# Optimization experiments

Hardware: AMD Instinct MI355X
Metric: run time of the kernel (lower is better)

The kernel has to match this reference:

```python
import jax, jax.numpy as jnp
import numpy as np
from jax.scipy.special import logsumexp

# config constants (match init_kwargs)
EPS_SH, IT_SH = 0.05, 10      # shared-space sinkhorn
EPS_AN, IT_AN = 0.05, 10      # anchor-space sinkhorn
TEMP_SAIL, BIAS_SAIL = 10.0, 0.0
CLAMP = 1e-8


def _rownorm(x):
    return x / jnp.clip(jnp.linalg.norm(x, axis=1, keepdims=True), CLAMP)


def cosine_similarity_matrix(a, b):
    return _rownorm(a) @ _rownorm(b).T


def sinkhorn(dist, epsilon, max_iter):
    """Log-domain Sinkhorn with uniform marginals. dist: (nx, ny)."""
    nx, ny = dist.shape
    M = -dist / epsilon                      # (nx, ny) log kernel
    log_a = -jnp.log(jnp.float32(nx))
    log_b = -jnp.log(jnp.float32(ny))

    def step(carry, _):
        u, v = carry
        u = log_a - logsumexp(M + v[None, :], axis=1)
        v = log_b - logsumexp(M + u[:, None], axis=0)
        return (u, v), None

    init = (jnp.zeros((nx,), M.dtype), jnp.zeros((ny,), M.dtype))
    (u, v), _ = jax.lax.scan(step, init, None, length=max_iter)
    log_plan = M + u[:, None] + v[None, :]
    return jnp.exp(log_plan), log_plan


def setup_inputs() -> dict:
    key = jax.random.key(0)
    ks = jax.random.split(key, 8)
    return {
        "fX_pairs": jax.random.normal(ks[0], (2048, 256), jnp.float32),
        "fY_pairs": jax.random.normal(ks[1], (2048, 256), jnp.float32),
        "X":        jax.random.normal(ks[2], (4096, 768), jnp.float32),
        "Y":        jax.random.normal(ks[3], (4096, 512), jnp.float32),
        "fX":       jax.random.normal(ks[4], (4096, 256), jnp.float32),
        "fY":       jax.random.normal(ks[5], (4096, 256), jnp.float32),
        "X_anchor": jax.random.normal(ks[6], (4096, 768), jnp.float32),
        "Y_anchor": jax.random.normal(ks[7], (4096, 512), jnp.float32),
    }


def _forward(fX_pairs, fY_pairs, X, Y, fX, fY, X_anchor, Y_anchor):
    # --- anchor covariances ---
    Xa, Ya = _rownorm(X_anchor), _rownorm(Y_anchor)
    Na = jnp.float32(Xa.shape[0])
    Sxx = (Xa.T @ Xa) / Na
    Syy = (Ya.T @ Ya) / Na
    Sxy = (Xa.T @ Ya) / Na

    # --- latent-space transport plans (shared sinkhorn) ---
    plan_p, logp_p = sinkhorn(-cosine_similarity_matrix(fX_pairs, fY_pairs), EPS_SH, IT_SH)
    plan_u, logp_u = sinkhorn(-cosine_similarity_matrix(fX, fY), EPS_SH, IT_SH)

    # --- marginal loss: marginals should be uniform ---
    def marginal_loss(plan):
        nx, ny = plan.shape
        a = jnp.full((nx,), 1.0 / nx, plan.dtype)
        b = jnp.full((ny,), 1.0 / ny, plan.dtype)
        return ((plan.sum(1) - a) ** 2).sum() + ((plan.sum(0) - b) ** 2).sum()

    L_marg = marginal_loss(plan_p) + marginal_loss(plan_u)

    # --- SAIL sigmoid contrastive loss on pairs ---
    N = fX_pairs.shape[0]
    cos = cosine_similarity_matrix(fX_pairs, fY_pairs)
    target = -1.0 + 2.0 * jnp.eye(N, dtype=cos.dtype)
    L_sail = -jnp.mean(jax.nn.log_sigmoid(cos * TEMP_SAIL * target - BIAS_SAIL))

    # --- supervised explicit: cosine distance on pairs ---
    L_exp = jnp.mean((1.0 - (_rownorm(fX_pairs) * _rownorm(fY_pairs)).sum(-1)) / 2.0)

    # --- supervised implicit: diag of log plan vs uniform identity ---
    L_imp = -jnp.mean(jnp.diag(logp_p) + jnp.log(jnp.float32(N)))

    # --- anchor-space plan (torch.no_grad -> stop_gradient) ---
    nX = jnp.clip(jnp.sqrt((X * (X @ Sxx)).sum(-1, keepdims=True)), CLAMP)
    nY = jnp.clip(jnp.sqrt((Y * (Y @ Syy)).sum(-1, keepdims=True)), CLAMP)
    Xn, Yn = X / nX, Y / nY
    plan_a, logp_a = jax.lax.stop_gradient(sinkhorn(-(Xn @ Sxy @ Yn.T), EPS_AN, IT_AN))
    Xn = jax.lax.stop_gradient(Xn)
    Yn = jax.lax.stop_gradient(Yn)

    # --- semisupervised OT: KL(plan_anchor || plan_latent) ---
    L_ot = (plan_a * (logp_a - logp_u)).sum()

    # --- semisupervised divergence (frobenius) ---
    fXn, fYn = _rownorm(fX), _rownorm(fY)
    norm1 = (((Xn.T @ Xn) @ Sxy @ (Yn.T @ Yn)) * Sxy).sum()
    norm2 = ((fXn.T @ fXn) * (fYn.T @ fYn)).sum()
    dot = (((Xn.T @ fXn) @ (fYn.T @ Yn)) * Sxy).sum()
    cste = jnp.float32(X.shape[0] * Y.shape[0])
    L_div = (norm1 + norm2 - 2.0 * dot) / cste

    # --- unsupervised Gromov-Wasserstein-style loss ---
    Xu = jax.lax.stop_gradient(_rownorm(X))
    Yu = jax.lax.stop_gradient(_rownorm(Y))
    Kx = Xu @ Xu.T   # (Nx, Nx)
    Ky = Yu @ Yu.T   # (Ny, Ny)
    a = plan_u.sum(1)
    b = plan_u.sum(0)
    L_gw = (a @ (Kx ** 2) @ a + b @ (Ky ** 2) @ b
            - 2.0 * ((Kx @ plan_u @ Ky) * plan_u).sum())

    return L_marg + L_sail + L_exp + L_imp + L_ot + L_div + L_gw


def reference(fX_pairs, fY_pairs, X, Y, fX, fY, X_anchor, Y_anchor):
    return _forward(fX_pairs, fY_pairs, X, Y, fX, fY, X_anchor, Y_anchor)
```

## Files before the change

### kernel.cpp

```cpp
#include <hip/hip_runtime.h>
#include <hip/hip_bf16.h>
#include <math.h>

using u16 = unsigned short;
using s8v = __attribute__((ext_vector_type(8))) short;
using s4v = __attribute__((ext_vector_type(4))) short;
using f4v = __attribute__((ext_vector_type(4))) float;

__device__ __forceinline__ float b2f(u16 x) {
    unsigned int u = ((unsigned int)x) << 16;
    return __uint_as_float(u);
}
__device__ __forceinline__ u16 f2b(float f) {
    unsigned int x = __float_as_uint(f);
    unsigned int r = x + 0x7fffu + ((x >> 16) & 1u);
    return (u16)(r >> 16);
}

__device__ __forceinline__ void a16(u16* lds, const u16* g) {
    __builtin_amdgcn_global_load_lds((__attribute__((address_space(1))) void*)g,
                                     (__attribute__((address_space(3))) void*)lds,
                                     16, 0, 0);
}

__device__ __forceinline__ float block_sum(float v, float* buf) {
    int t = threadIdx.x;
    buf[t] = v; __syncthreads();
    for (int s = 128; s > 0; s >>= 1) {
        if (t < s) buf[t] += buf[t + s];
        __syncthreads();
    }
    float r = buf[0];
    __syncthreads();
    return r;
}

__device__ __forceinline__ float wave_sum(float v) {
#pragma unroll
    for (int off = 32; off; off >>= 1) v += __shfl_xor(v, off, 64);
    return v;
}

__device__ __forceinline__ void block_atomic4(float wval, float* slot) {
    __shared__ float wb[4];
    int lane = threadIdx.x & 63, wv = threadIdx.x >> 6;
    if (lane == 0) wb[wv] = wval;
    __syncthreads();
    if (threadIdx.x == 0) atomicAdd(slot, wb[0] + wb[1] + wb[2] + wb[3]);
}

#define TBM 128
#define TBN 128
#define TBK 32

template<int EPI>
__global__ __launch_bounds__(256)
void gemm_bt(const u16* __restrict__ A, const u16* __restrict__ B,
             float* __restrict__ Cf, u16* __restrict__ Cb,
             int M, int N, int K, int ld, float alpha)
{
    __shared__ __align__(16) u16 As[TBM * TBK];
    __shared__ __align__(16) u16 Bs[TBN * TBK];

    const int tid  = threadIdx.x;
    const int lane = tid & 63;
    const int wave = tid >> 6;
    const int wm   = (wave >> 1) * 64;
    const int wn   = (wave & 1) * 64;
    const int l16  = lane & 15;
    const int q4   = lane >> 4;
    const size_t row0 = (size_t)blockIdx.y * TBM;
    const size_t col0 = (size_t)blockIdx.x * TBN;
    const int kOff = blockIdx.z * K;

    f4v acc[4][4];
#pragma unroll
    for (int mt = 0; mt < 4; ++mt)
#pragma unroll
        for (int nt = 0; nt < 4; ++nt)
#pragma unroll
            for (int r = 0; r < 4; ++r)
                acc[mt][nt][r] = 0.f;

    const int ar0 = wave * 32 + (lane >> 2);
    const int ar1 = ar0 + 16;
    const int akk = (lane & 3) * 8;
    const u16* gA0 = A + (row0 + ar0) * ld + kOff + akk;
    const u16* gA1 = A + (row0 + ar1) * ld + kOff + akk;
    const u16* gB0 = B + (col0 + ar0) * ld + kOff + akk;
    const u16* gB1 = B + (col0 + ar1) * ld + kOff + akk;
    u16* lA0 = As + wave * 1024;
    u16* lA1 = As + wave * 1024 + 512;
    u16* lB0 = Bs + wave * 1024;
    u16* lB1 = Bs + wave * 1024 + 512;

    for (int k0 = 0; k0 < K; k0 += TBK) {
        __syncthreads();
        a16(lA0, gA0 + k0);
        a16(lA1, gA1 + k0);
        a16(lB0, gB0 + k0);
        a16(lB1, gB1 + k0);
        __syncthreads();

        s8v af[4], bfr[4];
#pragma unroll
        for (int mt = 0; mt < 4; ++mt)
            af[mt] = *(const s8v*)(As + (wm + mt * 16 + l16) * TBK + q4 * 8);
#pragma unroll
        for (int nt = 0; nt < 4; ++nt)
            bfr[nt] = *(const s8v*)(Bs + (wn + nt * 16 + l16) * TBK + q4 * 8);
#pragma unroll
        for (int mt = 0; mt < 4; ++mt)
#pragma unroll
            for (int nt = 0; nt < 4; ++nt)
                acc[mt][nt] = __builtin_amdgcn_mfma_f32_16x16x32_bf16(af[mt], bfr[nt], acc[mt][nt], 0, 0, 0);
    }

#pragma unroll
    for (int mt = 0; mt < 4; ++mt)
#pragma unroll
        for (int nt = 0; nt < 4; ++nt)
#pragma unroll
            for (int r = 0; r < 4; ++r) {
                size_t row = row0 + wm + mt * 16 + q4 * 4 + r;
                size_t col = col0 + wn + nt * 16 + l16;
                float v = acc[mt][nt][r] * alpha;
                if (EPI == 1) Cb[row * (size_t)N + col] = f2b(v);
                else          atomicAdd(&Cf[row * (size_t)N + col], v);
            }
}

struct BGN {
    const u16* A; const u16* B;
    float* Cf; u16* Cb;
    const u16* W; float* slot;
    int M, N, Kc, ld, WL, tN, tEnd;
};
struct BGNArgs { BGN d[6]; int n; float alpha; };

template<int EPI>
__global__ __launch_bounds__(256)
void bgemmN(BGNArgs g)
{
    __shared__ __align__(16) u16 As[TBM * TBK];
    __shared__ __align__(16) u16 Bs[TBN * TBK];

    int bi = 0;
    while (bi < g.n - 1 && (int)blockIdx.x >= g.d[bi].tEnd) ++bi;
    const BGN& d = g.d[bi];
    const int tStart = bi ? g.d[bi - 1].tEnd : 0;
    const int local = blockIdx.x - tStart;
    const int tm = local / d.tN;
    const int tn = local - tm * d.tN;

    const int tid  = threadIdx.x;
    const int lane = tid & 63;
    const int wave = tid >> 6;
    const int wm   = (wave >> 1) * 64;
    const int wn   = (wave & 1) * 64;
    const int l16  = lane & 15;
    const int q4   = lane >> 4;
    const size_t row0 = (size_t)tm * TBM;
    const size_t col0 = (size_t)tn * TBN;
    const int kOff = blockIdx.y * d.Kc;
    const int ld = d.ld;

    f4v acc[4][4];
#pragma unroll
    for (int mt = 0; mt < 4; ++mt)
#pragma unroll
        for (int nt = 0; nt < 4; ++nt)
#pragma unroll
            for (int r = 0; r < 4; ++r)
                acc[mt][nt][r] = 0.f;

    const int ar0 = wave * 32 + (lane >> 2);
    const int ar1 = ar0 + 16;
    const int akk = (lane & 3) * 8;
    const u16* gA0 = d.A + (row0 + ar0) * ld + kOff + akk;
    const u16* gA1 = d.A + (row0 + ar1) * ld + kOff + akk;
    const u16* gB0 = d.B + (col0 + ar0) * ld + kOff + akk;
    const u16* gB1 = d.B + (col0 + ar1) * ld + kOff + akk;
    u16* lA0 = As + wave * 1024;
    u16* lA1 = As + wave * 1024 + 512;
    u16* lB0 = Bs + wave * 1024;
    u16* lB1 = Bs + wave * 1024 + 512;

    for (int k0 = 0; k0 < d.Kc; k0 += TBK) {
        __syncthreads();
        a16(lA0, gA0 + k0);
        a16(lA1, gA1 + k0);
        a16(lB0, gB0 + k0);
        a16(lB1, gB1 + k0);
        __syncthreads();

        s8v af[4], bfr[4];
#pragma unroll
        for (int mt = 0; mt < 4; ++mt)
            af[mt] = *(const s8v*)(As + (wm + mt * 16 + l16) * TBK + q4 * 8);
#pragma unroll
        for (int nt = 0; nt < 4; ++nt)
            bfr[nt] = *(const s8v*)(Bs + (wn + nt * 16 + l16) * TBK + q4 * 8);
#pragma unroll
        for (int mt = 0; mt < 4; ++mt)
#pragma unroll
            for (int nt = 0; nt < 4; ++nt)
                acc[mt][nt] = __builtin_amdgcn_mfma_f32_16x16x32_bf16(af[mt], bfr[nt], acc[mt][nt], 0, 0, 0);
    }

    if (EPI == 2) {
        float local2 = 0.f;
#pragma unroll
        for (int mt = 0; mt < 4; ++mt)
#pragma unroll
            for (int nt = 0; nt < 4; ++nt)
#pragma unroll
                for (int r = 0; r < 4; ++r) {
                    size_t row = row0 + wm + mt * 16 + q4 * 4 + r;
                    size_t col = col0 + wn + nt * 16 + l16;
                    local2 += acc[mt][nt][r] * b2f(d.W[col * (size_t)d.WL + row]);
                }
        __shared__ float red[256];
        float tot = block_sum(local2 * g.alpha, red);
        if (tid == 0) atomicAdd(d.slot, tot);
    } else {
#pragma unroll
        for (int mt = 0; mt < 4; ++mt)
#pragma unroll
            for (int nt = 0; nt < 4; ++nt)
#pragma unroll
                for (int r = 0; r < 4; ++r) {
                    size_t row = row0 + wm + mt * 16 + q4 * 4 + r;
                    size_t col = col0 + wn + nt * 16 + l16;
                    float v = acc[mt][nt][r] * g.alpha;
                    if (EPI == 0)      d.Cf[row * (size_t)d.N + col] = v;
                    else if (EPI == 1) d.Cb[row * (size_t)d.N + col] = f2b(v);
                    else               atomicAdd(&d.Cf[row * (size_t)d.N + col], v);
                }
    }
}

struct RN { const float* in; u16* out; int C; int rEnd; };
struct RNArgs { RN d[8]; int n; };

__global__ __launch_bounds__(256)
void rownorm_batch(RNArgs a) {
    int gw = (blockIdx.x * 256 + threadIdx.x) >> 6;
    int lane = threadIdx.x & 63;
    int i = 0;
    while (i < a.n - 1 && gw >= a.d[i].rEnd) ++i;
    if (gw >= a.d[i].rEnd) return;
    int row = gw - (i ? a.d[i - 1].rEnd : 0);
    int C = a.d[i].C;
    const float4* r4 = (const float4*)(a.d[i].in + (size_t)row * C);
    int nv = C >> 2;
    float ss = 0.f;
    for (int c = lane; c < nv; c += 64) {
        float4 v = r4[c];
        ss += v.x * v.x + v.y * v.y + v.z * v.z + v.w * v.w;
    }
    ss = wave_sum(ss);
    float inv = 1.f / fmaxf(sqrtf(ss), 1e-8f);
    s4v* o4 = (s4v*)(a.d[i].out + (size_t)row * C);
    for (int c = lane; c < nv; c += 64) {
        float4 v = r4[c];
        s4v o;
        o[0] = (short)f2b(v.x * inv); o[1] = (short)f2b(v.y * inv);
        o[2] = (short)f2b(v.z * inv); o[3] = (short)f2b(v.w * inv);
        o4[c] = o;
    }
}

__global__ __launch_bounds__(256)
void mahal_w(const u16* __restrict__ Xh, const float* __restrict__ XS,
             u16* __restrict__ out, int nrows, int C) {
    int row = (blockIdx.x * 256 + threadIdx.x) >> 6;
    int lane = threadIdx.x & 63;
    if (row >= nrows) return;
    const s4v* x4 = (const s4v*)(Xh + (size_t)row * C);
    const float4* s4 = (const float4*)(XS + (size_t)row * C);
    int nv = C >> 2;
    float s = 0.f;
    for (int c = lane; c < nv; c += 64) {
        s4v x = x4[c]; float4 v = s4[c];
        s += b2f((u16)x[0]) * v.x + b2f((u16)x[1]) * v.y
           + b2f((u16)x[2]) * v.z + b2f((u16)x[3]) * v.w;
    }
    s = wave_sum(s);
    float inv = 1.f / fmaxf(sqrtf(fmaxf(s, 0.f)), 1e-8f);
    s4v* o4 = (s4v*)(out + (size_t)row * C);
    for (int c = lane; c < nv; c += 64) {
        s4v x = x4[c], o;
#pragma unroll
        for (int k = 0; k < 4; ++k) o[k] = (short)f2b(b2f((u16)x[k]) * inv);
        o4[c] = o;
    }
}

struct TP { const u16* in; u16* out; int R, C, tC, tEnd; const float* s; };
struct TPArgs { TP d[6]; int n; };

__global__ __launch_bounds__(256)
void transpose_batch(TPArgs a) {
    __shared__ u16 tile[32][33];
    int t = blockIdx.x;
    int i = 0;
    while (i < a.n - 1 && t >= a.d[i].tEnd) ++i;
    int local = t - (i ? a.d[i - 1].tEnd : 0);
    const TP& d = a.d[i];
    int ty = local / d.tC, tx = local - ty * d.tC;
    int bx = tx * 32, by = ty * 32;
    int lx = threadIdx.x & 31;
    int lyy = threadIdx.x >> 5;
    for (int r = lyy; r < 32; r += 8)
        tile[r][lx] = d.in[(size_t)(by + r) * d.C + bx + lx];
    __syncthreads();
    for (int r = lyy; r < 32; r += 8) {
        u16 val = tile[lx][r];
        if (d.s) val = f2b(b2f(val) * d.s[by + lx]);
        d.out[(size_t)(bx + r) * d.R + by + lx] = val;
    }
}

__global__ __launch_bounds__(256)
void cast_f2b(const float* __restrict__ in, u16* __restrict__ out, int n) {
    for (int i = blockIdx.x * 256 + threadIdx.x; i < n; i += gridDim.x * 256)
        out[i] = f2b(in[i]);
}

__device__ __forceinline__ float row_sumexp(const u16* __restrict__ rowp,
                                            const float* __restrict__ vin,
                                            int ny, float scale, int lane) {
    const s8v* r8 = (const s8v*)rowp;
    const float4* v4 = (const float4*)vin;
    int nv = ny >> 3;
    float s = 0.f;
    for (int c = lane; c < nv; c += 64) {
        s8v v8 = r8[c];
        float4 va = v4[c * 2], vb = v4[c * 2 + 1];
        s += __expf(b2f((u16)v8[0]) * scale + va.x);
        s += __expf(b2f((u16)v8[1]) * scale + va.y);
        s += __expf(b2f((u16)v8[2]) * scale + va.z);
        s += __expf(b2f((u16)v8[3]) * scale + va.w);
        s += __expf(b2f((u16)v8[4]) * scale + vb.x);
        s += __expf(b2f((u16)v8[5]) * scale + vb.y);
        s += __expf(b2f((u16)v8[6]) * scale + vb.z);
        s += __expf(b2f((u16)v8[7]) * scale + vb.w);
    }
    return wave_sum(s);
}

__global__ __launch_bounds__(256)
void row_lse_tri(const u16* __restrict__ C1, const float* __restrict__ v1, float* __restrict__ u1,
                 const u16* __restrict__ C2, const float* __restrict__ v2, float* __restrict__ u2,
                 const u16* __restrict__ C3, const float* __restrict__ v3, float* __restrict__ u3,
                 float scale, float lm12, float lm3) {
    int gw = (blockIdx.x * 256 + threadIdx.x) >> 6;
    int lane = threadIdx.x & 63;
    if (gw < 4096) {
        float s = row_sumexp(C1 + (size_t)gw * 4096, v1, 4096, scale, lane);
        if (lane == 0) u1[gw] = lm12 - __logf(s);
    } else if (gw < 8192) {
        int row = gw - 4096;
        float s = row_sumexp(C2 + (size_t)row * 4096, v2, 4096, scale, lane);
        if (lane == 0) u2[row] = lm12 - __logf(s);
    } else {
        int row = gw - 8192;
        if (row >= 2048) return;
        float s = row_sumexp(C3 + (size_t)row * 2048, v3, 2048, scale, lane);
        if (lane == 0) u3[row] = lm3 - __logf(s);
    }
}

__device__ __forceinline__ float plan_body(const u16* __restrict__ rowp, u16* __restrict__ prow,
                                           float ui, const float* __restrict__ vin,
                                           int ny, float scale, int lane) {
    const s8v* r8 = (const s8v*)rowp;
    s8v* p8 = (s8v*)prow;
    const float4* v4 = (const float4*)vin;
    int nv = ny >> 3;
    float s = 0.f;
    for (int c = lane; c < nv; c += 64) {
        s8v v8 = r8[c], pb;
        float4 va = v4[c * 2], vb = v4[c * 2 + 1];
        float vv[8] = {va.x, va.y, va.z, va.w, vb.x, vb.y, vb.z, vb.w};
#pragma unroll
        for (int k = 0; k < 8; ++k) {
            float p = __expf(b2f((u16)v8[k]) * scale + ui + vv[k]);
            s += p;
            pb[k] = (short)f2b(p);
        }
        if (p8) p8[c] = pb;
    }
    return wave_sum(s);
}

__global__ __launch_bounds__(256)
void plan_quad(const u16* __restrict__ Cu, const u16* __restrict__ CuT,
               const u16* __restrict__ cosp, const u16* __restrict__ cospT,
               const float* __restrict__ uu, const float* __restrict__ vu,
               const float* __restrict__ up, const float* __restrict__ vp,
               u16* __restrict__ plan,
               float* __restrict__ au, float* __restrict__ bu,
               float* __restrict__ ap, float* __restrict__ bp, float scale) {
    int gw = (blockIdx.x * 256 + threadIdx.x) >> 6;
    int lane = threadIdx.x & 63;
    if (gw < 4096) {
        float s = plan_body(Cu + (size_t)gw * 4096, plan + (size_t)gw * 4096, uu[gw], vu, 4096, scale, lane);
        if (lane == 0) au[gw] = s;
    } else if (gw < 8192) {
        int r = gw - 4096;
        float s = plan_body(CuT + (size_t)r * 4096, nullptr, vu[r], uu, 4096, scale, lane);
        if (lane == 0) bu[r] = s;
    } else if (gw < 10240) {
        int r = gw - 8192;
        float s = plan_body(cosp + (size_t)r * 2048, nullptr, up[r], vp, 2048, scale, lane);
        if (lane == 0) ap[r] = s;
    } else {
        int r = gw - 10240;
        if (r >= 2048) return;
        float s = plan_body(cospT + (size_t)r * 2048, nullptr, vp[r], up, 2048, scale, lane);
        if (lane == 0) bp[r] = s;
    }
}

__global__ __launch_bounds__(256)
void marg4(const float* __restrict__ ap, const float* __restrict__ bp,
           const float* __restrict__ au, const float* __restrict__ bu,
           float* __restrict__ slot) {
    const float* sv; int n; float target;
    if (blockIdx.x == 0)      { sv = ap; n = 2048; target = 1.f / 2048.f; }
    else if (blockIdx.x == 1) { sv = bp; n = 2048; target = 1.f / 2048.f; }
    else if (blockIdx.x == 2) { sv = au; n = 4096; target = 1.f / 4096.f; }
    else                      { sv = bu; n = 4096; target = 1.f / 4096.f; }
    int t = threadIdx.x;
    float s = 0.f;
    for (int i = t; i < n; i += 256) { float d = sv[i] - target; s += d * d; }
    __shared__ float buf[256];
    float tot = block_sum(s, buf);
    if (t == 0) atomicAdd(slot, tot);
}

__global__ __launch_bounds__(256)
void ot_row_w(const u16* __restrict__ Ca, const u16* __restrict__ Cu,
              const float* __restrict__ ua, const float* __restrict__ va,
              const float* __restrict__ uu, const float* __restrict__ vu,
              int nrows, int ny, float scale, float* __restrict__ slot) {
    int row = (blockIdx.x * 256 + threadIdx.x) >> 6;
    int lane = threadIdx.x & 63;
    float local = 0.f;
    if (row < nrows) {
        const s8v* ra = (const s8v*)(Ca + (size_t)row * ny);
        const s8v* ru = (const s8v*)(Cu + (size_t)row * ny);
        const float4* va4 = (const float4*)va;
        const float4* vu4 = (const float4*)vu;
        float uai = ua[row], uui = uu[row];
        int nv = ny >> 3;
        for (int c = lane; c < nv; c += 64) {
            s8v a8 = ra[c], u8 = ru[c];
            float4 a0 = va4[c * 2], a1 = va4[c * 2 + 1];
            float4 u0 = vu4[c * 2], u1 = vu4[c * 2 + 1];
            float av[8] = {a0.x, a0.y, a0.z, a0.w, a1.x, a1.y, a1.z, a1.w};
            float uv[8] = {u0.x, u0.y, u0.z, u0.w, u1.x, u1.y, u1.z, u1.w};
#pragma unroll
            for (int k = 0; k < 8; ++k) {
                float lpa = b2f((u16)a8[k]) * scale + uai + av[k];
                float lpu = b2f((u16)u8[k]) * scale + uui + uv[k];
                local += __expf(lpa) * (lpa - lpu);
            }
        }
    }
    local = wave_sum(local);
    block_atomic4(local, slot);
}

__global__ __launch_bounds__(256)
void sail_row_w(const u16* __restrict__ cosb, int n, float temp, float* __restrict__ slot) {
    int row = (blockIdx.x * 256 + threadIdx.x) >> 6;
    int lane = threadIdx.x & 63;
    float local = 0.f;
    if (row < n) {
        const s8v* r8 = (const s8v*)(cosb + (size_t)row * n);
        int nv = n >> 3;
        for (int c = lane; c < nv; c += 64) {
            s8v v8 = r8[c];
#pragma unroll
            for (int k = 0; k < 8; ++k) {
                int j = c * 8 + k;
                float cv = b2f((u16)v8[k]);
                float wgt = cv * ((j == row) ? temp : -temp);
                local -= fminf(wgt, 0.f) - log1pf(__expf(-fabsf(wgt)));
            }
        }
    }
    local = wave_sum(local);
    block_atomic4(local, slot);
}

__global__ __launch_bounds__(256)
void diag2(const u16* __restrict__ cosb, const float* __restrict__ up,
           const float* __restrict__ vp, int n, float scale,
           float* __restrict__ slotExp, float* __restrict__ slotImp) {
    int t = threadIdx.x;
    float e = 0.f, im = 0.f;
    float logn = logf((float)n);
    for (int i = t; i < n; i += 256) {
        float c = b2f(cosb[(size_t)i * n + i]);
        e  += (1.f - c) * 0.5f;
        im += scale * c + up[i] + vp[i] + logn;
    }
    __shared__ float buf[256];
    float te = block_sum(e, buf);
    float ti = block_sum(im, buf);
    if (t == 0) { atomicAdd(slotExp, te); atomicAdd(slotImp, ti); }
}

__global__ __launch_bounds__(256)
void dot_bb(const u16* __restrict__ A, const u16* __restrict__ B, int n,
            float* __restrict__ slot) {
    int t = threadIdx.x;
    float local = 0.f;
    for (int i = blockIdx.x * 256 + t; i < n; i += gridDim.x * 256)
        local += b2f(A[i]) * b2f(B[i]);
    __shared__ float buf[256];
    float tot = block_sum(local, buf);
    if (t == 0) atomicAdd(slot, tot);
}

__global__ __launch_bounds__(256)
void dot3(const float* __restrict__ A, const float* __restrict__ B, const float* __restrict__ C,
          int na, int nb, int nc, float* __restrict__ sA, float* __restrict__ sB, float* __restrict__ sC) {
    const float* p; int n, b0, nblk; float* slot;
    if (blockIdx.x < 32)      { p = A; n = na; b0 = 0;  nblk = 32; slot = sA; }
    else if (blockIdx.x < 48) { p = B; n = nb; b0 = 32; nblk = 16; slot = sB; }
    else                      { p = C; n = nc; b0 = 48; nblk = 16; slot = sC; }
    int t = threadIdx.x;
    float local = 0.f;
    for (int i = (blockIdx.x - b0) * 256 + t; i < n; i += nblk * 256) {
        float v = p[i]; local += v * v;
    }
    __shared__ float buf[256];
    float tot = block_sum(local, buf);
    if (t == 0) atomicAdd(slot, tot);
}

__global__ void combine(const float* __restrict__ s, float* __restrict__ out) {
    if (threadIdx.x == 0 && blockIdx.x == 0) {
        float Np = 2048.f;
        float Nu2 = 4096.f * 4096.f;
        float total = s[0]
                    + s[1] / (Np * Np)
                    + s[2] / Np
                    - s[3] / Np
                    + s[4]
                    + (s[5] + s[6] - 2.f * s[7]) / Nu2
                    + s[8] + s[9] - 2.f * s[10];
        out[0] = total;
    }
}

extern "C" void kernel_launch(void* const* d_in, const int* in_sizes, int n_in,
                              void* d_out, int out_size, void* d_ws, size_t ws_size,
                              hipStream_t stream) {
    const float* fXp_in = (const float*)d_in[0];
    const float* fYp_in = (const float*)d_in[1];
    const float* X_in   = (const float*)d_in[2];
    const float* Y_in   = (const float*)d_in[3];
    const float* fX_in  = (const float*)d_in[4];
    const float* fY_in  = (const float*)d_in[5];
    const float* Xa_in  = (const float*)d_in[6];
    const float* Ya_in  = (const float*)d_in[7];
    float* out = (float*)d_out;

    char* w = (char*)d_ws;
    size_t off = 0;
    auto alloc = [&](size_t bytes) -> char* {
        char* p = w + off;
        off += (bytes + 255) & ~(size_t)255;
        return p;
    };

    const size_t N = 4096, Np = 2048, DX = 768, DY = 512, DF = 256;

    const size_t SLOT = N * N * 2;
    char* S1 = alloc(SLOT);
    char* S2 = alloc(SLOT);
    char* S3 = alloc(SLOT);
    char* S4 = alloc(SLOT);
    char* S5 = alloc(SLOT);

    u16* Xa   = (u16*)S1;
    u16* Cu   = (u16*)S1;
    u16* T1T  = (u16*)S1;
    u16* Ya   = (u16*)S2;
    u16* CuT  = (u16*)S2;
    u16* XuT  = (u16*)S2;
    u16* YuT  = (u16*)(S2 + N * DX * 2);
    u16* Ca   = (u16*)S3;
    u16* XsT  = (u16*)S3;
    u16* YsT  = (u16*)(S3 + N * DX * 2);
    u16* XaT  = (u16*)S4;
    u16* YaT  = (u16*)(S4 + N * DX * 2);
    float* XS = (float*)S4;
    u16* XnT  = (u16*)S4;
    u16* YnT  = (u16*)(S4 + N * DX * 2);
    u16* CaT  = (u16*)S4;
    float* T1F= (float*)S4;
    float* YS = (float*)S5;
    u16* Tb   = (u16*)S5;
    u16* plan = (u16*)S5;

    u16* fXp  = (u16*)alloc(Np * DF * 2);
    u16* fYp  = (u16*)alloc(Np * DF * 2);
    u16* fXn  = (u16*)alloc(N * DF * 2);
    u16* fYn  = (u16*)alloc(N * DF * 2);
    u16* fXnT = (u16*)alloc(N * DF * 2);
    u16* fYnT = (u16*)alloc(N * DF * 2);
    u16* Xu   = (u16*)alloc(N * DX * 2);
    u16* Yu   = (u16*)alloc(N * DY * 2);
    u16* Xn   = (u16*)alloc(N * DX * 2);
    u16* Yn   = (u16*)alloc(N * DY * 2);
    u16* Sxx  = (u16*)alloc(DX * DX * 2);
    u16* Syy  = (u16*)alloc(DY * DY * 2);
    u16* SxyT = (u16*)alloc(DY * DX * 2);
    u16* Gx   = (u16*)alloc(DX * DX * 2);
    u16* Gy   = (u16*)alloc(DY * DY * 2);
    u16* Gfx  = (u16*)alloc(DF * DF * 2);
    u16* Gfy  = (u16*)alloc(DF * DF * 2);
    u16* A1b  = (u16*)alloc(DX * DF * 2);
    u16* B1Tb = (u16*)alloc(DY * DF * 2);
    u16* Hb   = (u16*)alloc(DX * DY * 2);
    u16* cosp = (u16*)alloc(Np * Np * 2);
    u16* cospT= (u16*)alloc(Np * Np * 2);
    float* ap = (float*)alloc(Np * 4);
    float* bp = (float*)alloc(Np * 4);
    float* au = (float*)alloc(N * 4);
    float* bu = (float*)alloc(N * 4);

    char* zero_begin = w + off;
    float* slots = (float*)alloc(64 * 4);
    float* up = (float*)alloc(Np * 4);
    float* vp = (float*)alloc(Np * 4);
    float* uu = (float*)alloc(N * 4);
    float* vu = (float*)alloc(N * 4);
    float* ua = (float*)alloc(N * 4);
    float* va = (float*)alloc(N * 4);
    float* SxxF  = (float*)alloc(DX * DX * 4);
    float* SyyF  = (float*)alloc(DY * DY * 4);
    float* SxyTF = (float*)alloc(DY * DX * 4);
    float* GxF   = (float*)alloc(DX * DX * 4);
    float* GyF   = (float*)alloc(DY * DY * 4);
    float* GfxF  = (float*)alloc(DF * DF * 4);
    float* GfyF  = (float*)alloc(DF * DF * 4);
    float* A1F   = (float*)alloc(DX * DF * 4);
    float* B1F   = (float*)alloc(DY * DF * 4);
    float* HbF   = (float*)alloc(DX * DY * 4);
    float* W1F   = (float*)alloc(DX * DX * 4);
    float* W2F   = (float*)alloc(DY * DY * 4);
    float* MF    = (float*)alloc(DX * DY * 4);
    size_t zero_bytes = (size_t)((w + off) - zero_begin);

    const float SCALE = 20.f;

    hipMemsetAsync(zero_begin, 0, zero_bytes, stream);

    {
        RNArgs a;
        a.d[0] = {Xa_in, Xa, 768, 4096};
        a.d[1] = {Ya_in, Ya, 512, 8192};
        a.d[2] = {fXp_in, fXp, 256, 10240};
        a.d[3] = {fYp_in, fYp, 256, 12288};
        a.d[4] = {fX_in, fXn, 256, 16384};
        a.d[5] = {fY_in, fYn, 256, 20480};
        a.d[6] = {X_in, Xu, 768, 24576};
        a.d[7] = {Y_in, Yu, 512, 28672};
        a.n = 8;
        rownorm_batch<<<7168, 256, 0, stream>>>(a);
    }

    {
        TPArgs a;
        a.d[0] = {Xa, XaT, 4096, 768, 24, 3072, nullptr};
        a.d[1] = {Ya, YaT, 4096, 512, 16, 5120, nullptr};
        a.d[2] = {fXn, fXnT, 4096, 256, 8, 6144, nullptr};
        a.d[3] = {fYn, fYnT, 4096, 256, 8, 7168, nullptr};
        a.n = 4;
        transpose_batch<<<7168, 256, 0, stream>>>(a);
    }

    {
        BGNArgs g;
        g.d[0] = {XaT, XaT, SxxF, nullptr, nullptr, nullptr, 768, 768, 512, 4096, 0, 6, 36};
        g.d[1] = {YaT, YaT, SyyF, nullptr, nullptr, nullptr, 512, 512, 512, 4096, 0, 4, 52};
        g.d[2] = {YaT, XaT, SxyTF, nullptr, nullptr, nullptr, 512, 768, 512, 4096, 0, 6, 76};
        g.n = 3; g.alpha = 1.f / 4096.f;
        bgemmN<3><<<dim3(76, 8), 256, 0, stream>>>(g);
        cast_f2b<<<256, 256, 0, stream>>>(SxxF, Sxx, 768 * 768 + 512 * 512 + 512 * 768);
    }

    {
        BGNArgs g;
        g.d[0] = {Xu, Sxx, XS, nullptr, nullptr, nullptr, 4096, 768, 768, 768, 0, 6, 192};
        g.d[1] = {Yu, Syy, YS, nullptr, nullptr, nullptr, 4096, 512, 512, 512, 0, 4, 320};
        g.n = 2; g.alpha = 1.f;
        bgemmN<0><<<dim3(320, 1), 256, 0, stream>>>(g);
    }
    mahal_w<<<1024, 256, 0, stream>>>(Xu, XS, Xn, 4096, 768);
    mahal_w<<<1024, 256, 0, stream>>>(Yu, YS, Yn, 4096, 512);

    {
        TPArgs a;
        a.d[0] = {Xn, XnT, 4096, 768, 24, 3072, nullptr};
        a.d[1] = {Yn, YnT, 4096, 512, 16, 5120, nullptr};
        a.n = 2;
        transpose_batch<<<5120, 256, 0, stream>>>(a);
    }

    {
        BGNArgs g;
        g.d[0] = {XnT, XnT, GxF, nullptr, nullptr, nullptr, 768, 768, 512, 4096, 0, 6, 36};
        g.d[1] = {YnT, YnT, GyF, nullptr, nullptr, nullptr, 512, 512, 512, 4096, 0, 4, 52};
        g.d[2] = {fXnT, fXnT, GfxF, nullptr, nullptr, nullptr, 256, 256, 512, 4096, 0, 2, 56};
        g.d[3] = {fYnT, fYnT, GfyF, nullptr, nullptr, nullptr, 256, 256, 512, 4096, 0, 2, 60};
        g.d[4] = {XnT, fXnT, A1F, nullptr, nullptr, nullptr, 768, 256, 512, 4096, 0, 2, 72};
        g.d[5] = {YnT, fYnT, B1F, nullptr, nullptr, nullptr, 512, 256, 512, 4096, 0, 2, 80};
        g.n = 6; g.alpha = 1.f;
        bgemmN<3><<<dim3(80, 8), 256, 0, stream>>>(g);
        cast_f2b<<<256, 256, 0, stream>>>(GxF, Gx,
            768 * 768 + 512 * 512 + 256 * 256 + 256 * 256 + 768 * 256 + 512 * 256);
    }

    {
        BGNArgs g;
        g.d[0] = {fXn, fYn, nullptr, Cu, nullptr, nullptr, 4096, 4096, 256, 256, 0, 32, 1024};
        g.d[1] = {fXp, fYp, nullptr, cosp, nullptr, nullptr, 2048, 2048, 256, 256, 0, 16, 1280};
        g.d[2] = {Xn, SxyT, nullptr, Tb, nullptr, nullptr, 4096, 512, 768, 768, 0, 4, 1408};
        g.n = 3; g.alpha = 1.f;
        bgemmN<1><<<dim3(1408, 1), 256, 0, stream>>>(g);
    }
    gemm_bt<1><<<dim3(32, 32), 256, 0, stream>>>(Tb, Yn, nullptr, Ca, 4096, 4096, 512, 512, 1.f);

    {
        TPArgs a;
        a.d[0] = {Cu, CuT, 4096, 4096, 128, 16384, nullptr};
        a.d[1] = {cosp, cospT, 2048, 2048, 64, 20480, nullptr};
        a.d[2] = {Ca, CaT, 4096, 4096, 128, 36864, nullptr};
        a.n = 3;
        transpose_batch<<<36864, 256, 0, stream>>>(a);
    }

    gemm_bt<3><<<dim3(4, 6, 4), 256, 0, stream>>>(Gx, SxyT, HbF, nullptr, 768, 512, 192, 768, 1.f);
    cast_f2b<<<256, 256, 0, stream>>>(HbF, Hb, 768 * 512);
    {
        BGNArgs g;
        g.d[0] = {Hb, Gy, nullptr, nullptr, SxyT, slots + 5, 768, 512, 128, 512, 768, 4, 24};
        g.d[1] = {A1b, B1Tb, nullptr, nullptr, SxyT, slots + 7, 768, 512, 64, 256, 768, 4, 48};
        g.n = 2; g.alpha = 1.f;
        bgemmN<2><<<dim3(48, 4), 256, 0, stream>>>(g);
    }
    dot_bb<<<64, 256, 0, stream>>>(Gfx, Gfy, 256 * 256, slots + 6);

    {
        float lm12 = -logf(4096.f), lm3 = -logf(2048.f);
        for (int it = 0; it < 10; ++it) {
            row_lse_tri<<<2560, 256, 0, stream>>>(Cu, vu, uu, Ca, va, ua, cosp, vp, up, SCALE, lm12, lm3);
            row_lse_tri<<<2560, 256, 0, stream>>>(CuT, uu, vu, CaT, ua, va, cospT, up, vp, SCALE, lm12, lm3);
        }
    }

    plan_quad<<<3072, 256, 0, stream>>>(Cu, CuT, cosp, cospT, uu, vu, up, vp,
                                        plan, au, bu, ap, bp, SCALE);
    marg4<<<4, 256, 0, stream>>>(ap, bp, au, bu, slots + 0);
    diag2<<<1, 256, 0, stream>>>(cosp, up, vp, 2048, SCALE, slots + 2, slots + 3);
    sail_row_w<<<512, 256, 0, stream>>>(cosp, 2048, 10.f, slots + 1);

    ot_row_w<<<1024, 256, 0, stream>>>(Ca, Cu, ua, va, uu, vu, 4096, 4096, SCALE, slots + 4);

    {
        TPArgs a;
        a.d[0] = {Xu, XuT, 4096, 768, 24, 3072, nullptr};
        a.d[1] = {Yu, YuT, 4096, 512, 16, 5120, nullptr};
        a.d[2] = {Xu, XsT, 4096, 768, 24, 8192, au};
        a.d[3] = {Yu, YsT, 4096, 512, 16, 10240, bu};
        a.n = 4;
        transpose_batch<<<10240, 256, 0, stream>>>(a);
    }
    hipMemsetAsync(T1F, 0, 512 * 4096 * 4, stream);
    {
        BGNArgs g;
        g.d[0] = {YuT, plan, T1F, nullptr, nullptr, nullptr, 512, 4096, 512, 4096, 0, 32, 128};
        g.d[1] = {XsT, XuT, W1F, nullptr, nullptr, nullptr, 768, 768, 512, 4096, 0, 6, 164};
        g.d[2] = {YsT, YuT, W2F, nullptr, nullptr, nullptr, 512, 512, 512, 4096, 0, 4, 180};
        g.n = 3; g.alpha = 1.f;
        bgemmN<3><<<dim3(180, 8), 256, 0, stream>>>(g);
    }
    cast_f2b<<<512, 256, 0, stream>>>(T1F, T1T, 512 * 4096);
    {
        BGNArgs g;
        g.d[0] = {XuT, T1T, MF, nullptr, nullptr, nullptr, 768, 512, 512, 4096, 0, 4, 24};
        g.n = 1; g.alpha = 1.f;
        bgemmN<3><<<dim3(24, 8), 256, 0, stream>>>(g);
    }
    dot3<<<64, 256, 0, stream>>>(W1F, W2F, MF, 768 * 768, 512 * 512, 768 * 512,
                                 slots + 8, slots + 9, slots + 10);

    combine<<<1, 1, 0, stream>>>(slots, out);
}
```

Baseline: 917.2 us.

## Fuse plan and OT passes, drop column marginals, split-K GEMMs into partial buffers

Merges the unsupervised plan computation with the OT KL row reduction so Cu is read once, and drops the column-sum passes over CuT/cospT along with their marginal terms. The GW split-K GEMMs now write per-slice partial results (new EPI 4) instead of atomically accumulating into a zeroed buffer. A new reduction kernel sums the partials, casts T1 to bf16 and computes the squared norms. The W2 path uses YuT directly with a 1/4096 scale rather than a b-weighted transpose. This assumes uniform column marginals (b = 1/N after the final v update), which holds for Sinkhorn ending on a v step, but it changes how the exact marginal error is computed and may be numerically approximate.

```diff
diff --git a/kernel.cpp b/kernel.cpp
--- a/kernel.cpp
+++ b/kernel.cpp
@@ -224,6 +224,7 @@
         float tot = block_sum(local2 * g.alpha, red);
         if (tid == 0) atomicAdd(d.slot, tot);
     } else {
+        float* Cs = (EPI == 4) ? d.Cf + (size_t)blockIdx.y * d.M * d.N : d.Cf;
 #pragma unroll
         for (int mt = 0; mt < 4; ++mt)
 #pragma unroll
@@ -235,6 +236,7 @@
                     float v = acc[mt][nt][r] * g.alpha;
                     if (EPI == 0)      d.Cf[row * (size_t)d.N + col] = v;
                     else if (EPI == 1) d.Cb[row * (size_t)d.N + col] = f2b(v);
+                    else if (EPI == 4) Cs[row * (size_t)d.N + col] = v;
                     else               atomicAdd(&d.Cf[row * (size_t)d.N + col], v);
                 }
     }
@@ -372,106 +374,77 @@
     }
 }
 
-__device__ __forceinline__ float plan_body(const u16* __restrict__ rowp, u16* __restrict__ prow,
-                                           float ui, const float* __restrict__ vin,
-                                           int ny, float scale, int lane) {
-    const s8v* r8 = (const s8v*)rowp;
-    s8v* p8 = (s8v*)prow;
-    const float4* v4 = (const float4*)vin;
-    int nv = ny >> 3;
-    float s = 0.f;
-    for (int c = lane; c < nv; c += 64) {
-        s8v v8 = r8[c], pb;
-        float4 va = v4[c * 2], vb = v4[c * 2 + 1];
-        float vv[8] = {va.x, va.y, va.z, va.w, vb.x, vb.y, vb.z, vb.w};
-#pragma unroll
-        for (int k = 0; k < 8; ++k) {
-            float p = __expf(b2f((u16)v8[k]) * scale + ui + vv[k]);
-            s += p;
-            pb[k] = (short)f2b(p);
-        }
-        if (p8) p8[c] = pb;
-    }
-    return wave_sum(s);
-}
-
-__global__ __launch_bounds__(256)
-void plan_quad(const u16* __restrict__ Cu, const u16* __restrict__ CuT,
-               const u16* __restrict__ cosp, const u16* __restrict__ cospT,
-               const float* __restrict__ uu, const float* __restrict__ vu,
-               const float* __restrict__ up, const float* __restrict__ vp,
-               u16* __restrict__ plan,
-               float* __restrict__ au, float* __restrict__ bu,
-               float* __restrict__ ap, float* __restrict__ bp, float scale) {
+__global__ __launch_bounds__(256)
+void plan_ot(const u16* __restrict__ Cu, const u16* __restrict__ Ca,
+             const u16* __restrict__ cosp,
+             const float* __restrict__ uu, const float* __restrict__ vu,
+             const float* __restrict__ ua, const float* __restrict__ va,
+             const float* __restrict__ up, const float* __restrict__ vp,
+             u16* __restrict__ plan,
+             float* __restrict__ au, float* __restrict__ ap,
+             float* __restrict__ slotOt, float scale) {
     int gw = (blockIdx.x * 256 + threadIdx.x) >> 6;
     int lane = threadIdx.x & 63;
-    if (gw < 4096) {
-        float s = plan_body(Cu + (size_t)gw * 4096, plan + (size_t)gw * 4096, uu[gw], vu, 4096, scale, lane);
-        if (lane == 0) au[gw] = s;
-    } else if (gw < 8192) {
+    if (blockIdx.x < 1024) {
+        int i = gw;
+        const s8v* ru = (const s8v*)(Cu + (size_t)i * 4096);
+        const s8v* ra = (const s8v*)(Ca + (size_t)i * 4096);
+        s8v* p8 = (s8v*)(plan + (size_t)i * 4096);
+        const float4* vu4 = (const float4*)vu;
+        const float4* va4 = (const float4*)va;
+        float uui = uu[i], uai = ua[i];
+        float sa = 0.f, ot = 0.f;
+        for (int c = lane; c < 512; c += 64) {
+            s8v u8 = ru[c], a8 = ra[c], pb;
+            float4 u0 = vu4[c * 2], u1 = vu4[c * 2 + 1];
+            float4 a0 = va4[c * 2], a1 = va4[c * 2 + 1];
+            float uv[8] = {u0.x, u0.y, u0.z, u0.w, u1.x, u1.y, u1.z, u1.w};
+            float av[8] = {a0.x, a0.y, a0.z, a0.w, a1.x, a1.y, a1.z, a1.w};
+#pragma unroll
+            for (int k = 0; k < 8; ++k) {
+                float lpu = b2f((u16)u8[k]) * scale + uui + uv[k];
+                float p = __expf(lpu);
+                sa += p;
+                pb[k] = (short)f2b(p);
+                float lpa = b2f((u16)a8[k]) * scale + uai + av[k];
+                ot += __expf(lpa) * (lpa - lpu);
+            }
+            p8[c] = pb;
+        }
+        sa = wave_sum(sa);
+        if (lane == 0) au[i] = sa;
+        ot = wave_sum(ot);
+        block_atomic4(ot, slotOt);
+    } else {
         int r = gw - 4096;
-        float s = plan_body(CuT + (size_t)r * 4096, nullptr, vu[r], uu, 4096, scale, lane);
-        if (lane == 0) bu[r] = s;
-    } else if (gw < 10240) {
-        int r = gw - 8192;
-        float s = plan_body(cosp + (size_t)r * 2048, nullptr, up[r], vp, 2048, scale, lane);
+        const s8v* r8 = (const s8v*)(cosp + (size_t)r * 2048);
+        const float4* vp4 = (const float4*)vp;
+        float ui = up[r], s = 0.f;
+        for (int c = lane; c < 256; c += 64) {
+            s8v v8 = r8[c];
+            float4 v0 = vp4[c * 2], v1 = vp4[c * 2 + 1];
+            float vv[8] = {v0.x, v0.y, v0.z, v0.w, v1.x, v1.y, v1.z, v1.w};
+#pragma unroll
+            for (int k = 0; k < 8; ++k)
+                s += __expf(b2f((u16)v8[k]) * scale + ui + vv[k]);
+        }
+        s = wave_sum(s);
         if (lane == 0) ap[r] = s;
-    } else {
-        int r = gw - 10240;
-        if (r >= 2048) return;
-        float s = plan_body(cospT + (size_t)r * 2048, nullptr, vp[r], up, 2048, scale, lane);
-        if (lane == 0) bp[r] = s;
-    }
-}
-
-__global__ __launch_bounds__(256)
-void marg4(const float* __restrict__ ap, const float* __restrict__ bp,
-           const float* __restrict__ au, const float* __restrict__ bu,
+    }
+}
+
+__global__ __launch_bounds__(256)
+void marg2(const float* __restrict__ ap, const float* __restrict__ au,
            float* __restrict__ slot) {
     const float* sv; int n; float target;
-    if (blockIdx.x == 0)      { sv = ap; n = 2048; target = 1.f / 2048.f; }
-    else if (blockIdx.x == 1) { sv = bp; n = 2048; target = 1.f / 2048.f; }
-    else if (blockIdx.x == 2) { sv = au; n = 4096; target = 1.f / 4096.f; }
-    else                      { sv = bu; n = 4096; target = 1.f / 4096.f; }
+    if (blockIdx.x == 0) { sv = ap; n = 2048; target = 1.f / 2048.f; }
+    else                 { sv = au; n = 4096; target = 1.f / 4096.f; }
     int t = threadIdx.x;
     float s = 0.f;
     for (int i = t; i < n; i += 256) { float d = sv[i] - target; s += d * d; }
     __shared__ float buf[256];
     float tot = block_sum(s, buf);
     if (t == 0) atomicAdd(slot, tot);
-}
-
-__global__ __launch_bounds__(256)
-void ot_row_w(const u16* __restrict__ Ca, const u16* __restrict__ Cu,
-              const float* __restrict__ ua, const float* __restrict__ va,
-              const float* __restrict__ uu, const float* __restrict__ vu,
-              int nrows, int ny, float scale, float* __restrict__ slot) {
-    int row = (blockIdx.x * 256 + threadIdx.x) >> 6;
-    int lane = threadIdx.x & 63;
-    float local = 0.f;
-    if (row < nrows) {
-        const s8v* ra = (const s8v*)(Ca + (size_t)row * ny);
-        const s8v* ru = (const s8v*)(Cu + (size_t)row * ny);
-        const float4* va4 = (const float4*)va;
-        const float4* vu4 = (const float4*)vu;
-        float uai = ua[row], uui = uu[row];
-        int nv = ny >> 3;
-        for (int c = lane; c < nv; c += 64) {
-            s8v a8 = ra[c], u8 = ru[c];
-            float4 a0 = va4[c * 2], a1 = va4[c * 2 + 1];
-            float4 u0 = vu4[c * 2], u1 = vu4[c * 2 + 1];
-            float av[8] = {a0.x, a0.y, a0.z, a0.w, a1.x, a1.y, a1.z, a1.w};
-            float uv[8] = {u0.x, u0.y, u0.z, u0.w, u1.x, u1.y, u1.z, u1.w};
-#pragma unroll
-            for (int k = 0; k < 8; ++k) {
-                float lpa = b2f((u16)a8[k]) * scale + uai + av[k];
-                float lpu = b2f((u16)u8[k]) * scale + uui + uv[k];
-                local += __expf(lpa) * (lpa - lpu);
-            }
-        }
-    }
-    local = wave_sum(local);
-    block_atomic4(local, slot);
 }
 
 __global__ __launch_bounds__(256)
@@ -528,15 +501,43 @@
 }
 
 __global__ __launch_bounds__(256)
-void dot3(const float* __restrict__ A, const float* __restrict__ B, const float* __restrict__ C,
-          int na, int nb, int nc, float* __restrict__ sA, float* __restrict__ sB, float* __restrict__ sC) {
-    const float* p; int n, b0, nblk; float* slot;
-    if (blockIdx.x < 32)      { p = A; n = na; b0 = 0;  nblk = 32; slot = sA; }
-    else if (blockIdx.x < 48) { p = B; n = nb; b0 = 32; nblk = 16; slot = sB; }
-    else                      { p = C; n = nc; b0 = 48; nblk = 16; slot = sC; }
+void gw_reduce(const float* __restrict__ T1S, u16* __restrict__ T1T,
+               const float* __restrict__ W1S, const float* __restrict__ W2S,
+               float* __restrict__ s8, float* __restrict__ s9) {
+    int b = blockIdx.x, t = threadIdx.x;
+    if (b < 512) {
+        const int n = 512 * 4096, st = n;
+        for (int i = b * 256 + t; i < n; i += 512 * 256)
+            T1T[i] = f2b(T1S[i] + T1S[i + st] + T1S[i + 2 * st] + T1S[i + 3 * st]);
+    } else if (b < 548) {
+        const int n = 768 * 768, st = n;
+        float local = 0.f;
+        for (int i = (b - 512) * 256 + t; i < n; i += 36 * 256) {
+            float v = W1S[i] + W1S[i + st] + W1S[i + 2 * st] + W1S[i + 3 * st];
+            local += v * v;
+        }
+        __shared__ float buf[256];
+        float tot = block_sum(local, buf);
+        if (t == 0) atomicAdd(s8, tot);
+    } else {
+        const int n = 512 * 512, st = n;
+        const float sc = 1.f / 4096.f;
+        float local = 0.f;
+        for (int i = (b - 548) * 256 + t; i < n; i += 16 * 256) {
+            float v = (W2S[i] + W2S[i + st] + W2S[i + 2 * st] + W2S[i + 3 * st]) * sc;
+            local += v * v;
+        }
+        __shared__ float buf[256];
+        float tot = block_sum(local, buf);
+        if (t == 0) atomicAdd(s9, tot);
+    }
+}
+
+__global__ __launch_bounds__(256)
+void sumsq(const float* __restrict__ p, int n, float* __restrict__ slot) {
     int t = threadIdx.x;
     float local = 0.f;
-    for (int i = (blockIdx.x - b0) * 256 + t; i < n; i += nblk * 256) {
+    for (int i = blockIdx.x * 256 + t; i < n; i += gridDim.x * 256) {
         float v = p[i]; local += v * v;
     }
     __shared__ float buf[256];
@@ -598,14 +599,15 @@
     u16* YuT  = (u16*)(S2 + N * DX * 2);
     u16* Ca   = (u16*)S3;
     u16* XsT  = (u16*)S3;
-    u16* YsT  = (u16*)(S3 + N * DX * 2);
+    float* W1S = (float*)(S3 + 8 * 1024 * 1024);
+    float* W2S = (float*)(S3 + 20 * 1024 * 1024);
     u16* XaT  = (u16*)S4;
     u16* YaT  = (u16*)(S4 + N * DX * 2);
     float* XS = (float*)S4;
     u16* XnT  = (u16*)S4;
     u16* YnT  = (u16*)(S4 + N * DX * 2);
     u16* CaT  = (u16*)S4;
-    float* T1F= (float*)S4;
+    float* T1S= (float*)S4;
     float* YS = (float*)S5;
     u16* Tb   = (u16*)S5;
     u16* plan = (u16*)S5;
@@ -633,9 +635,7 @@
     u16* cosp = (u16*)alloc(Np * Np * 2);
     u16* cospT= (u16*)alloc(Np * Np * 2);
     float* ap = (float*)alloc(Np * 4);
-    float* bp = (float*)alloc(Np * 4);
     float* au = (float*)alloc(N * 4);
-    float* bu = (float*)alloc(N * 4);
 
     char* zero_begin = w + off;
     float* slots = (float*)alloc(64 * 4);
@@ -655,8 +655,6 @@
     float* A1F   = (float*)alloc(DX * DF * 4);
     float* B1F   = (float*)alloc(DY * DF * 4);
     float* HbF   = (float*)alloc(DX * DY * 4);
-    float* W1F   = (float*)alloc(DX * DX * 4);
-    float* W2F   = (float*)alloc(DY * DY * 4);
     float* MF    = (float*)alloc(DX * DY * 4);
     size_t zero_bytes = (size_t)((w + off) - zero_begin);
 
@@ -768,41 +766,36 @@
         }
     }
 
-    plan_quad<<<3072, 256, 0, stream>>>(Cu, CuT, cosp, cospT, uu, vu, up, vp,
-                                        plan, au, bu, ap, bp, SCALE);
-    marg4<<<4, 256, 0, stream>>>(ap, bp, au, bu, slots + 0);
+    plan_ot<<<1536, 256, 0, stream>>>(Cu, Ca, cosp, uu, vu, ua, va, up, vp,
+                                      plan, au, ap, slots + 4, SCALE);
+    marg2<<<2, 256, 0, stream>>>(ap, au, slots + 0);
     diag2<<<1, 256, 0, stream>>>(cosp, up, vp, 2048, SCALE, slots + 2, slots + 3);
     sail_row_w<<<512, 256, 0, stream>>>(cosp, 2048, 10.f, slots + 1);
-
-    ot_row_w<<<1024, 256, 0, stream>>>(Ca, Cu, ua, va, uu, vu, 4096, 4096, SCALE, slots + 4);
 
     {
         TPArgs a;
         a.d[0] = {Xu, XuT, 4096, 768, 24, 3072, nullptr};
         a.d[1] = {Yu, YuT, 4096, 512, 16, 5120, nullptr};
         a.d[2] = {Xu, XsT, 4096, 768, 24, 8192, au};
-        a.d[3] = {Yu, YsT, 4096, 512, 16, 10240, bu};
-        a.n = 4;
-        transpose_batch<<<10240, 256, 0, stream>>>(a);
-    }
-    hipMemsetAsync(T1F, 0, 512 * 4096 * 4, stream);
+        a.n = 3;
+        transpose_batch<<<8192, 256, 0, stream>>>(a);
+    }
     {
         BGNArgs g;
-        g.d[0] = {YuT, plan, T1F, nullptr, nullptr, nullptr, 512, 4096, 512, 4096, 0, 32, 128};
-        g.d[1] = {XsT, XuT, W1F, nullptr, nullptr, nullptr, 768, 768, 512, 4096, 0, 6, 164};
-        g.d[2] = {YsT, YuT, W2F, nullptr, nullptr, nullptr, 512, 512, 512, 4096, 0, 4, 180};
+        g.d[0] = {YuT, plan, T1S, nullptr, nullptr, nullptr, 512, 4096, 1024, 4096, 0, 32, 128};
+        g.d[1] = {XsT, XuT, W1S, nullptr, nullptr, nullptr, 768, 768, 1024, 4096, 0, 6, 164};
+        g.d[2] = {YuT, YuT, W2S, nullptr, nullptr, nullptr, 512, 512, 1024, 4096, 0, 4, 180};
         g.n = 3; g.alpha = 1.f;
-        bgemmN<3><<<dim3(180, 8), 256, 0, stream>>>(g);
-    }
-    cast_f2b<<<512, 256, 0, stream>>>(T1F, T1T, 512 * 4096);
+        bgemmN<4><<<dim3(180, 4), 256, 0, stream>>>(g);
+    }
+    gw_reduce<<<564, 256, 0, stream>>>(T1S, T1T, W1S, W2S, slots + 8, slots + 9);
     {
         BGNArgs g;
         g.d[0] = {XuT, T1T, MF, nullptr, nullptr, nullptr, 768, 512, 512, 4096, 0, 4, 24};
         g.n = 1; g.alpha = 1.f;
         bgemmN<3><<<dim3(24, 8), 256, 0, stream>>>(g);
     }
-    dot3<<<64, 256, 0, stream>>>(W1F, W2F, MF, 768 * 768, 512 * 512, 768 * 512,
-                                 slots + 8, slots + 9, slots + 10);
+    sumsq<<<32, 256, 0, stream>>>(MF, 768 * 512, slots + 10);
 
     combine<<<1, 1, 0, stream>>>(slots, out);
 }
```

New measurement: 847.7 us. -7.6%, faster.
